# Optimization experiments

Measured on AMD Instinct MI355X. Metric: run time of the kernel, lower is better.

Reference implementation:

```python
import jax, jax.numpy as jnp
import numpy as np

BLKQ = 64
BLKK = 64
TOPK_RATIO = 0.25
EPS = 1e-05


def mean_pool(x, blk):
    B, H, L, D = x.shape
    return x.reshape(B, H, L // blk, blk, D).mean(axis=3)


def setup_inputs() -> dict:
    key = jax.random.key(0)
    kq, kk, kv, kw, kb = jax.random.split(key, 5)
    B, H, Lq, Lk, D = 1, 8, 4096, 4096, 64
    q = jax.random.normal(kq, (B, H, Lq, D), dtype=jnp.float32)
    k = jax.random.normal(kk, (B, H, Lk, D), dtype=jnp.float32)
    v = jax.random.normal(kv, (B, H, Lk, D), dtype=jnp.float32)
    # proj_l is zero-initialized in the original; use small random weights so the
    # linear-attention branch contributes non-trivially to the output.
    proj_w = jax.random.normal(kw, (D, D), dtype=jnp.float32) * 0.02
    proj_b = jax.random.normal(kb, (D,), dtype=jnp.float32) * 0.02
    return {"q": q, "k": k, "v": v, "proj_w": proj_w, "proj_b": proj_b}


def reference(q, k, v, proj_w, proj_b):
    B, H, Lq, D = q.shape
    Lk = k.shape[2]
    nQ, nK = Lq // BLKQ, Lk // BLKK

    # ---- block-level top-k routing (get_block_map_cross) ----
    arg_k = k - k.mean(axis=-2, keepdims=True)
    pq = mean_pool(q, BLKQ)                      # (B,H,nQ,D)
    pk = mean_pool(arg_k, BLKK)                  # (B,H,nK,D)
    pooled_score = jnp.einsum('bhqd,bhkd->bhqk', pq, pk)  # (B,H,nQ,nK)
    topk = min(nK, max(1, int(TOPK_RATIO * nK)))
    lut = jax.lax.top_k(pooled_score, topk)[1]   # (B,H,nQ,topk) int32

    # ---- block-sparse cross attention (softmax over selected K blocks) ----
    qb = q.reshape(B, H, nQ, BLKQ, D)
    kb = k.reshape(B, H, nK, BLKK, D)
    vb = v.reshape(B, H, nK, BLKK, D)
    gather = jax.vmap(jax.vmap(lambda blocks, idx: blocks[idx]))  # over B,H
    kg = gather(kb, lut)                         # (B,H,nQ,topk,BLKK,D)
    vg = gather(vb, lut)                         # (B,H,nQ,topk,BLKK,D)
    scale = D ** -0.5
    s = jnp.einsum('bhnqd,bhntkd->bhnqtk', qb, kg) * scale
    s = s.reshape(B, H, nQ, BLKQ, topk * BLKK)
    p = jax.nn.softmax(s, axis=-1)
    o_s = jnp.einsum('bhnqt,bhntd->bhnqd', p, vg.reshape(B, H, nQ, topk * BLKK, D))
    o_s = o_s.reshape(B, H, Lq, D)

    # ---- linear attention branch (softmax feature map, tied q/k) ----
    qf = jax.nn.softmax(q, axis=-1)
    kf = jax.nn.softmax(k, axis=-1)
    kv = jnp.einsum('bhkd,bhke->bhde', kf, v)    # (B,H,D,D)
    denom = jnp.einsum('bhqd,bhd->bhq', qf, kf.sum(axis=2)) + EPS
    o_l = jnp.einsum('bhqd,bhde->bhqe', qf, kv) / denom[..., None]
    o_l = o_l @ proj_w.T + proj_b                # proj_l

    return o_s + o_l
```

## Files before the change

kernel.cpp:

```cpp
#include <hip/hip_runtime.h>
#include <math.h>

#define H 8
#define L 4096
#define D 64
#define NBLK 64
#define TOPK 16
#define EPS 1e-5f
#define LP 68

typedef unsigned short u16;
typedef unsigned int u32;
typedef __attribute__((ext_vector_type(8))) short bf16x8;
typedef __attribute__((ext_vector_type(16))) float f32x16;
typedef __attribute__((ext_vector_type(4))) u32 u32x4;

static __device__ __forceinline__ u16 f2bf(float x) {
  u32 u = __float_as_uint(x);
  u32 r = (u + 0x7fffu + ((u >> 16) & 1u)) >> 16;
  return (u16)r;
}
static __device__ __forceinline__ float bf2f(u16 h) {
  return __uint_as_float(((u32)h) << 16);
}
__device__ __forceinline__ float dot4f(float4 a, float4 b) {
  return a.x * b.x + a.y * b.y + a.z * b.z + a.w * b.w;
}

__global__ __launch_bounds__(256) void kvprep_kernel(
    const float* __restrict__ k, const float* __restrict__ v,
    u16* __restrict__ kpkb, u16* __restrict__ vpkb,
    float* __restrict__ pkp, float* __restrict__ part_kv,
    float* __restrict__ part_ks) {
  const int kb = blockIdx.x, h = blockIdx.y;
  __shared__ float kst[64 * LP];
  __shared__ float vst[64 * LP];
  __shared__ float red[4][64];
  const int t = threadIdx.x;

  {
    const float4* ksrc = (const float4*)(k + ((size_t)h * L + (size_t)kb * 64) * D);
    const float4* vsrc = (const float4*)(v + ((size_t)h * L + (size_t)kb * 64) * D);
#pragma unroll
    for (int i = 0; i < 4; ++i) {
      int flat = i * 256 + t;
      int row = flat >> 4, c4 = flat & 15;
      *(float4*)&kst[row * LP + c4 * 4] = ksrc[flat];
      *(float4*)&vst[row * LP + c4 * 4] = vsrc[flat];
    }
  }
  __syncthreads();

  {
    u16* rowbase = kpkb + ((size_t)h * L + (size_t)kb * 64) * 128;
#pragma unroll
    for (int pass = 0; pass < 2; ++pass) {
      const int key = pass * 32 + (t >> 3);
      const int sub = t & 7;
      float f[8];
#pragma unroll
      for (int e = 0; e < 8; ++e) f[e] = kst[key * LP + sub * 8 + e];
      u16 hi[8], lo[8];
#pragma unroll
      for (int e = 0; e < 8; ++e) {
        hi[e] = f2bf(f[e]);
        lo[e] = f2bf(f[e] - bf2f(hi[e]));
      }
      const int c = sub >> 1, g2 = sub & 1;
      u16* row = rowbase + (size_t)key * 128;
      const int sh = ((c * 4 + g2 * 2 + 0) ^ (key & 15)) * 8;
      const int sl = ((c * 4 + g2 * 2 + 1) ^ (key & 15)) * 8;
      uint4 vh = {(u32)hi[0] | ((u32)hi[1] << 16), (u32)hi[2] | ((u32)hi[3] << 16),
                  (u32)hi[4] | ((u32)hi[5] << 16), (u32)hi[6] | ((u32)hi[7] << 16)};
      uint4 vl = {(u32)lo[0] | ((u32)lo[1] << 16), (u32)lo[2] | ((u32)lo[3] << 16),
                  (u32)lo[4] | ((u32)lo[5] << 16), (u32)lo[6] | ((u32)lo[7] << 16)};
      *(uint4*)(row + sh) = vh;
      *(uint4*)(row + sl) = vl;
    }
  }

  {
    const int d = t & 63, rr = t >> 6;
    float s = 0.f;
#pragma unroll
    for (int i = 0; i < 16; ++i) s += kst[(rr * 16 + i) * LP + d];
    red[rr][d] = s;
  }
  __syncthreads();
  {
    const int d = t & 63, rr = t >> 6;
    if (rr == 0) {
      float tot = red[0][d] + red[1][d] + red[2][d] + red[3][d];
      pkp[((size_t)h * NBLK + kb) * D + d] = tot * (1.f / 64.f);
    }
  }

  {
    u16* base = vpkb + (((size_t)h * 64 + kb) * 64) * 128;
#pragma unroll
    for (int iter = 0; iter < 4; ++iter) {
      const int dim = iter * 16 + (t >> 4);
      const int s = t & 15;
      const int cgh = s ^ (dim & 15);
      const int c = cgh >> 2, g = (cgh >> 1) & 1, hl = cgh & 1;
      u16 o[8];
#pragma unroll
      for (int e = 0; e < 8; ++e) {
        const int key = 4 * g + (e & 3) + 8 * ((e >> 2) + 2 * (c & 1)) + 32 * (c >> 1);
        float val = vst[key * LP + dim];
        u16 hi = f2bf(val);
        o[e] = hl ? f2bf(val - bf2f(hi)) : hi;
      }
      uint4 pk4 = {(u32)o[0] | ((u32)o[1] << 16), (u32)o[2] | ((u32)o[3] << 16),
                   (u32)o[4] | ((u32)o[5] << 16), (u32)o[6] | ((u32)o[7] << 16)};
      *(uint4*)(base + (size_t)dim * 128 + s * 8) = pk4;
    }
  }

  if (t < 128) {
    const int row = t >> 1, half = t & 1;
    float4 kr[8];
#pragma unroll
    for (int i = 0; i < 8; ++i) kr[i] = *(float4*)&kst[row * LP + half * 32 + i * 4];
    float mxk = -INFINITY;
#pragma unroll
    for (int i = 0; i < 8; ++i)
      mxk = fmaxf(mxk, fmaxf(fmaxf(kr[i].x, kr[i].y), fmaxf(kr[i].z, kr[i].w)));
    mxk = fmaxf(mxk, __shfl_xor(mxk, 1));
    float smk = 0.f;
#pragma unroll
    for (int i = 0; i < 8; ++i) {
      kr[i].x = __expf(kr[i].x - mxk); kr[i].y = __expf(kr[i].y - mxk);
      kr[i].z = __expf(kr[i].z - mxk); kr[i].w = __expf(kr[i].w - mxk);
      smk += kr[i].x + kr[i].y + kr[i].z + kr[i].w;
    }
    smk += __shfl_xor(smk, 1);
    const float inv = 1.f / smk;
#pragma unroll
    for (int i = 0; i < 8; ++i) {
      float4 o = kr[i];
      o.x *= inv; o.y *= inv; o.z *= inv; o.w *= inv;
      *(float4*)&kst[row * LP + half * 32 + i * 4] = o;
    }
  }
  __syncthreads();

  {
    const int d = t & 63, eg = t >> 6;
    float4 acc0 = make_float4(0.f, 0.f, 0.f, 0.f);
    float4 acc1 = acc0, acc2 = acc0, acc3 = acc0;
    float ksacc = 0.f;
#pragma unroll 4
    for (int lr = 0; lr < 64; ++lr) {
      const float wv = kst[lr * LP + d];
      if (eg == 0) ksacc += wv;
      const float4* vr = (const float4*)&vst[lr * LP + eg * 16];
      float4 v0 = vr[0], v1 = vr[1], v2 = vr[2], v3 = vr[3];
      acc0.x += wv * v0.x; acc0.y += wv * v0.y; acc0.z += wv * v0.z; acc0.w += wv * v0.w;
      acc1.x += wv * v1.x; acc1.y += wv * v1.y; acc1.z += wv * v1.z; acc1.w += wv * v1.w;
      acc2.x += wv * v2.x; acc2.y += wv * v2.y; acc2.z += wv * v2.z; acc2.w += wv * v2.w;
      acc3.x += wv * v3.x; acc3.y += wv * v3.y; acc3.z += wv * v3.z; acc3.w += wv * v3.w;
    }
    float* kvb = part_kv + ((size_t)(h * 64 + kb)) * 4096 + (size_t)d * 64 + eg * 16;
    *(float4*)(kvb + 0) = acc0;
    *(float4*)(kvb + 4) = acc1;
    *(float4*)(kvb + 8) = acc2;
    *(float4*)(kvb + 12) = acc3;
    if (eg == 0) part_ks[(size_t)(h * 64 + kb) * 64 + d] = ksacc;
  }
}

__global__ __launch_bounds__(256) void pool_kernel(
    const float* __restrict__ src, float* __restrict__ dst) {
  const int blk = blockIdx.x, h = blockIdx.y;
  const int d = threadIdx.x & 63, rr = threadIdx.x >> 6;
  const float* base = src + ((size_t)h * L + (size_t)blk * 64) * D;
  float s = 0.f;
#pragma unroll
  for (int i = 0; i < 16; ++i) s += base[(rr * 16 + i) * D + d];
  __shared__ float red[4][64];
  red[rr][d] = s;
  __syncthreads();
  if (rr == 0) {
    float tot = red[0][d] + red[1][d] + red[2][d] + red[3][d];
    dst[((size_t)h * NBLK + blk) * D + d] = tot * (1.f / 64.f);
  }
}

__global__ __launch_bounds__(64) void topk_kernel(
    const float* __restrict__ pq, const float* __restrict__ pk,
    int* __restrict__ lut) {
  const int qb = blockIdx.x, h = blockIdx.y;
  const int j = threadIdx.x;
  const float4* pqv = (const float4*)(pq + ((size_t)h * NBLK + qb) * D);
  const float4* pkv = (const float4*)(pk + ((size_t)h * NBLK + j) * D);
  float s = 0.f;
#pragma unroll
  for (int d4 = 0; d4 < 16; ++d4) s += dot4f(pqv[d4], pkv[d4]);
  int* lrow = lut + ((size_t)h * NBLK + qb) * TOPK;
  for (int t = 0; t < TOPK; ++t) {
    float m = s;
    int mi = j;
#pragma unroll
    for (int off = 32; off; off >>= 1) {
      float om = __shfl_xor(m, off);
      int omi = __shfl_xor(mi, off);
      if (om > m || (om == m && omi < mi)) { m = om; mi = omi; }
    }
    if (j == 0) lrow[t] = mi;
    if (j == mi) s = -INFINITY;
  }
}

__global__ __launch_bounds__(256, 4) void sattn_kernel(
    const float* __restrict__ q, const u16* __restrict__ kpk,
    const u16* __restrict__ vpk, const int* __restrict__ lut,
    float* __restrict__ out) {
  __shared__ alignas(16) char smem[32768];
  const int bx = blockIdx.x;
  const int h = bx & 7, qb = bx >> 3;
  const int t = threadIdx.x;
  const int lane = t & 63;
  const int ln = lane & 31;
  const int g = lane >> 5;
  const int w = t >> 6;
  const int p = w & 1;
  const int kh = w >> 1;

  float* qst = (float*)smem;
  {
    const float4* src = (const float4*)(q + ((size_t)h * L + (size_t)qb * 64) * D);
#pragma unroll
    for (int i = 0; i < 4; ++i) {
      int flat = i * 256 + t;
      *(float4*)&qst[(flat >> 4) * LP + (flat & 15) * 4] = src[flat];
    }
  }
  __syncthreads();
  bf16x8 qh[4], ql[4];
  {
    const int qrow = p * 32 + ln;
#pragma unroll
    for (int c = 0; c < 4; ++c) {
      const float* s8 = &qst[qrow * LP + c * 16 + g * 8];
#pragma unroll
      for (int e = 0; e < 8; ++e) {
        float x = s8[e] * 0.125f;
        u16 hi = f2bf(x);
        qh[c][e] = (short)hi;
        ql[c][e] = (short)f2bf(x - bf2f(hi));
      }
    }
  }
  __syncthreads();

  u16* KB = (u16*)smem;
  u16* VB = (u16*)smem + 8192;

  f32x16 o0, o1;
#pragma unroll
  for (int r = 0; r < 16; ++r) { o0[r] = 0.f; o1[r] = 0.f; }
  float lrun = 0.f;
  const int* lrow = lut + ((size_t)h * NBLK + qb) * TOPK;
  const int xr = ln & 15;
  const int krow = kh * 32 + ln;

  {
    const int kb = lrow[0];
    const uint4* gk = (const uint4*)(kpk + ((size_t)h * L + (size_t)kb * 64) * 128);
    const uint4* gv = (const uint4*)(vpk + (((size_t)h * 64 + kb) * 64) * 128);
    uint4* lk = (uint4*)KB;
    uint4* lv = (uint4*)VB;
#pragma unroll
    for (int i = 0; i < 4; ++i) {
      int x = i * 256 + t;
      lk[x] = gk[x];
      lv[x] = gv[x];
    }
  }
  __syncthreads();

  for (int ib = 0; ib < TOPK; ++ib) {
    f32x16 s0;
#pragma unroll
    for (int r = 0; r < 16; ++r) s0[r] = 0.f;
#pragma unroll
    for (int c = 0; c < 4; ++c) {
      const int sH = c * 4 + g * 2;
      bf16x8 k_h = *(const bf16x8*)(KB + (size_t)krow * 128 + ((sH ^ xr) * 8));
      bf16x8 k_l = *(const bf16x8*)(KB + (size_t)krow * 128 + (((sH + 1) ^ xr) * 8));
      s0 = __builtin_amdgcn_mfma_f32_32x32x16_bf16(k_h, qh[c], s0, 0, 0, 0);
      s0 = __builtin_amdgcn_mfma_f32_32x32x16_bf16(k_l, qh[c], s0, 0, 0, 0);
      s0 = __builtin_amdgcn_mfma_f32_32x32x16_bf16(k_h, ql[c], s0, 0, 0, 0);
    }

    u32 hpk[8], lpk[8];
    float psum = 0.f;
#pragma unroll
    for (int j = 0; j < 8; ++j) {
      float a = __expf(s0[2 * j]);
      float b = __expf(s0[2 * j + 1]);
      psum += a + b;
      u32 hp;
      asm("v_cvt_pk_bf16_f32 %0, %1, %2" : "=v"(hp) : "v"(a), "v"(b));
      hpk[j] = hp;
      float ah = __uint_as_float(hp << 16);
      float bh = __uint_as_float(hp & 0xffff0000u);
      u32 lp;
      asm("v_cvt_pk_bf16_f32 %0, %1, %2" : "=v"(lp) : "v"(a - ah), "v"(b - bh));
      lpk[j] = lp;
    }
    psum += __shfl_xor(psum, 32);
    lrun += psum;

#pragma unroll
    for (int cc = 0; cc < 2; ++cc) {
      union { u32x4 u; bf16x8 b; } ph, pl;
      ph.u = (u32x4){hpk[4 * cc + 0], hpk[4 * cc + 1], hpk[4 * cc + 2], hpk[4 * cc + 3]};
      pl.u = (u32x4){lpk[4 * cc + 0], lpk[4 * cc + 1], lpk[4 * cc + 2], lpk[4 * cc + 3]};
      const bf16x8 pah = ph.b, pal = pl.b;
      const int sH = (2 * kh + cc) * 4 + g * 2;
      bf16x8 v0h = *(const bf16x8*)(VB + (size_t)ln * 128 + ((sH ^ xr) * 8));
      bf16x8 v0l = *(const bf16x8*)(VB + (size_t)ln * 128 + (((sH + 1) ^ xr) * 8));
      bf16x8 v1h = *(const bf16x8*)(VB + (size_t)(32 + ln) * 128 + ((sH ^ xr) * 8));
      bf16x8 v1l = *(const bf16x8*)(VB + (size_t)(32 + ln) * 128 + (((sH + 1) ^ xr) * 8));
      o0 = __builtin_amdgcn_mfma_f32_32x32x16_bf16(pah, v0h, o0, 0, 0, 0);
      o0 = __builtin_amdgcn_mfma_f32_32x32x16_bf16(pal, v0h, o0, 0, 0, 0);
      o0 = __builtin_amdgcn_mfma_f32_32x32x16_bf16(pah, v0l, o0, 0, 0, 0);
      o1 = __builtin_amdgcn_mfma_f32_32x32x16_bf16(pah, v1h, o1, 0, 0, 0);
      o1 = __builtin_amdgcn_mfma_f32_32x32x16_bf16(pal, v1h, o1, 0, 0, 0);
      o1 = __builtin_amdgcn_mfma_f32_32x32x16_bf16(pah, v1l, o1, 0, 0, 0);
    }

    __syncthreads();
    if (ib + 1 < TOPK) {
      const int kb = lrow[ib + 1];
      const uint4* gk = (const uint4*)(kpk + ((size_t)h * L + (size_t)kb * 64) * 128);
      const uint4* gv = (const uint4*)(vpk + (((size_t)h * 64 + kb) * 64) * 128);
      uint4* lk = (uint4*)KB;
      uint4* lv = (uint4*)VB;
#pragma unroll
      for (int i = 0; i < 4; ++i) {
        int x = i * 256 + t;
        lk[x] = gk[x];
        lv[x] = gv[x];
      }
    }
    __syncthreads();
  }

  float* oxbase = (float*)smem;
  float* lxbase = (float*)smem + 4096;
  if (g == 0) lxbase[(p * 2 + kh) * 32 + ln] = lrun;
  if (kh == 1) {
#pragma unroll
    for (int r = 0; r < 16; ++r) {
      const int R = (r & 3) + 8 * (r >> 2) + 4 * g;
      oxbase[p * 2048 + R * 64 + ln] = o0[r];
      oxbase[p * 2048 + R * 64 + 32 + ln] = o1[r];
    }
  }
  __syncthreads();
  if (kh == 0) {
#pragma unroll
    for (int r = 0; r < 16; ++r) {
      const int R = (r & 3) + 8 * (r >> 2) + 4 * g;
      const float lt = lxbase[(p * 2 + 0) * 32 + R] + lxbase[(p * 2 + 1) * 32 + R];
      const float inv = 1.f / lt;
      const size_t row = (size_t)h * L + (size_t)qb * 64 + p * 32 + R;
      out[row * 64 + ln] = (o0[r] + oxbase[p * 2048 + R * 64 + ln]) * inv;
      out[row * 64 + 32 + ln] = (o1[r] + oxbase[p * 2048 + R * 64 + 32 + ln]) * inv;
    }
  }
}

__global__ __launch_bounds__(256) void kvred_kernel(
    const float* __restrict__ part_kv, const float* __restrict__ part_ks,
    float* __restrict__ p2kv, float* __restrict__ p2ks) {
  const int j = blockIdx.x, h = blockIdx.y;
  const int t = threadIdx.x;
  float4 s0 = make_float4(0.f, 0.f, 0.f, 0.f);
  float4 s1 = s0, s2 = s0, s3 = s0;
#pragma unroll
  for (int p = 0; p < 4; ++p) {
    const float4* src = (const float4*)(part_kv + ((size_t)(h * 64 + j * 4 + p)) * 4096);
    float4 a = src[0 * 256 + t], b = src[1 * 256 + t];
    float4 c = src[2 * 256 + t], d = src[3 * 256 + t];
    s0.x += a.x; s0.y += a.y; s0.z += a.z; s0.w += a.w;
    s1.x += b.x; s1.y += b.y; s1.z += b.z; s1.w += b.w;
    s2.x += c.x; s2.y += c.y; s2.z += c.z; s2.w += c.w;
    s3.x += d.x; s3.y += d.y; s3.z += d.z; s3.w += d.w;
  }
  float4* dst = (float4*)(p2kv + ((size_t)(h * 16 + j)) * 4096);
  dst[0 * 256 + t] = s0;
  dst[1 * 256 + t] = s1;
  dst[2 * 256 + t] = s2;
  dst[3 * 256 + t] = s3;
  if (t < 64) {
    float ks = 0.f;
#pragma unroll
    for (int p = 0; p < 4; ++p) ks += part_ks[(size_t)(h * 64 + j * 4 + p) * 64 + t];
    p2ks[(size_t)(h * 16 + j) * 64 + t] = ks;
  }
}

__global__ __launch_bounds__(256) void kvproj_kernel(
    const float* __restrict__ p2kv, const float* __restrict__ p2ks,
    const float* __restrict__ pw, float* __restrict__ kvp,
    float* __restrict__ ksum) {
  const int h = blockIdx.x;
  __shared__ float kvs[64 * 64];
  __shared__ float pws[64 * 64];
  const int t = threadIdx.x;
  float4 s0 = make_float4(0.f, 0.f, 0.f, 0.f);
  float4 s1 = s0, s2 = s0, s3 = s0;
  for (int p = 0; p < 16; ++p) {
    const float4* src = (const float4*)(p2kv + ((size_t)(h * 16 + p)) * 4096);
    float4 a = src[0 * 256 + t], b = src[1 * 256 + t];
    float4 cc = src[2 * 256 + t], dd = src[3 * 256 + t];
    s0.x += a.x; s0.y += a.y; s0.z += a.z; s0.w += a.w;
    s1.x += b.x; s1.y += b.y; s1.z += b.z; s1.w += b.w;
    s2.x += cc.x; s2.y += cc.y; s2.z += cc.z; s2.w += cc.w;
    s3.x += dd.x; s3.y += dd.y; s3.z += dd.z; s3.w += dd.w;
  }
  ((float4*)kvs)[0 * 256 + t] = s0;
  ((float4*)kvs)[1 * 256 + t] = s1;
  ((float4*)kvs)[2 * 256 + t] = s2;
  ((float4*)kvs)[3 * 256 + t] = s3;
#pragma unroll
  for (int i = 0; i < 4; ++i) {
    int f4 = i * 256 + t;
    ((float4*)pws)[f4] = ((const float4*)pw)[f4];
  }
  if (t < 64) {
    float ks = 0.f;
    for (int p = 0; p < 16; ++p) ks += p2ks[(size_t)(h * 16 + p) * 64 + t];
    ksum[(size_t)h * 64 + t] = ks;
  }
  __syncthreads();
  const int d = t & 63, fg = t >> 6;
  float* dst = kvp + (size_t)h * 4096 + (size_t)d * 64;
  const float4* a = (const float4*)&kvs[d * 64];
  for (int f = fg * 16; f < fg * 16 + 16; ++f) {
    const float4* b = (const float4*)&pws[f * 64];
    float s = 0.f;
#pragma unroll
    for (int e4 = 0; e4 < 16; ++e4) s += dot4f(a[e4], b[e4]);
    dst[f] = s;
  }
}

__global__ __launch_bounds__(256) void linattn_kernel(
    const float* __restrict__ q, const float* __restrict__ kvp,
    const float* __restrict__ ksum, const float* __restrict__ pb,
    float* __restrict__ out) {
  __shared__ float kvs[64 * 64];
  __shared__ float kss[64], pbs[64];
  const int t = threadIdx.x;
  const size_t grow = (size_t)blockIdx.x * 256 + t;
  const int h = (int)(grow >> 12);
#pragma unroll
  for (int i = 0; i < 4; ++i) {
    int f4 = i * 256 + t;
    ((float4*)kvs)[f4] = ((const float4*)(kvp + (size_t)h * 4096))[f4];
  }
  if (t < 64) {
    kss[t] = ksum[(size_t)h * 64 + t];
    pbs[t] = pb[t];
  }
  __syncthreads();
  const float* qrow = q + grow * 64;
  float mx = -INFINITY;
  const float4* q4p = (const float4*)qrow;
#pragma unroll
  for (int i = 0; i < 16; ++i) {
    float4 x = q4p[i];
    mx = fmaxf(mx, fmaxf(fmaxf(x.x, x.y), fmaxf(x.z, x.w)));
  }
  float4 tt[16];
#pragma unroll
  for (int i = 0; i < 16; ++i) tt[i] = make_float4(0.f, 0.f, 0.f, 0.f);
  float sm = 0.f, dn = 0.f;
#pragma unroll 4
  for (int dd = 0; dd < 64; ++dd) {
    const float wv = __expf(qrow[dd] - mx);
    sm += wv;
    dn += wv * kss[dd];
    const float4* kvr = (const float4*)&kvs[dd * 64];
#pragma unroll
    for (int e4 = 0; e4 < 16; ++e4) {
      float4 kk = kvr[e4];
      tt[e4].x += wv * kk.x; tt[e4].y += wv * kk.y;
      tt[e4].z += wv * kk.z; tt[e4].w += wv * kk.w;
    }
  }
  const float inv = 1.f / (dn + EPS * sm);
  float* orow = out + grow * 64;
#pragma unroll
  for (int e4 = 0; e4 < 16; ++e4) {
    float4 o = ((float4*)orow)[e4];
    o.x += tt[e4].x * inv + pbs[e4 * 4 + 0];
    o.y += tt[e4].y * inv + pbs[e4 * 4 + 1];
    o.z += tt[e4].z * inv + pbs[e4 * 4 + 2];
    o.w += tt[e4].w * inv + pbs[e4 * 4 + 3];
    ((float4*)orow)[e4] = o;
  }
}

extern "C" void kernel_launch(void* const* d_in, const int* in_sizes, int n_in,
                              void* d_out, int out_size, void* d_ws, size_t ws_size,
                              hipStream_t stream) {
  const float* q = (const float*)d_in[0];
  const float* k = (const float*)d_in[1];
  const float* v = (const float*)d_in[2];
  const float* pw = (const float*)d_in[3];
  const float* pb = (const float*)d_in[4];
  float* out = (float*)d_out;

  u16* kpkb = (u16*)d_ws;
  u16* vpkb = (u16*)d_ws + 4194304;
  float* fws = (float*)((char*)d_ws + 16777216);
  float* pq = fws;
  float* pk = fws + 32768;
  float* part_kv = fws + 65536;
  float* part_ks = fws + 2162688;
  float* p2kv = fws + 2195456;
  float* p2ks = fws + 2719744;
  float* kvp = fws + 2727936;
  float* ksum = fws + 2760704;
  int* lut = (int*)(fws + 2761216);

  kvprep_kernel<<<dim3(64, 8), 256, 0, stream>>>(k, v, kpkb, vpkb, pk, part_kv, part_ks);
  pool_kernel<<<dim3(64, 8), 256, 0, stream>>>(q, pq);
  topk_kernel<<<dim3(64, 8), 64, 0, stream>>>(pq, pk, lut);
  sattn_kernel<<<512, 256, 0, stream>>>(q, kpkb, vpkb, lut, out);
  kvred_kernel<<<dim3(16, 8), 256, 0, stream>>>(part_kv, part_ks, p2kv, p2ks);
  kvproj_kernel<<<8, 256, 0, stream>>>(p2kv, p2ks, pw, kvp, ksum);
  linattn_kernel<<<128, 256, 0, stream>>>(q, kvp, ksum, pb, out);
}
```

Measured before the change: 177.2 us.

## Double-buffer K/V blocks with async global-to-LDS loads in sparse attention

The sparse-attention kernel now prefetches the next selected K/V block into a second LDS buffer with async global_load_lds copies while the current block is computed, replacing the load-then-compute pattern that used two barriers per step. LDS per block doubles to 64KB and the launch-bounds occupancy hint drops from 4 to 2 blocks. It also loads Q straight from global memory into registers instead of staging it through LDS, and raises wave priority around the MFMA sections. This lowers achievable occupancy, though with 512 blocks on the device that may already be near the actual residency.

Result: faster. 172.0 us (-2.9%).

```diff
diff --git a/kernel.cpp b/kernel.cpp
--- a/kernel.cpp
+++ b/kernel.cpp
@@ -25,6 +25,11 @@
 }
 __device__ __forceinline__ float dot4f(float4 a, float4 b) {
   return a.x * b.x + a.y * b.y + a.z * b.z + a.w * b.w;
+}
+static __device__ __forceinline__ void async_cp16(uint4* lds, const uint4* g) {
+  __builtin_amdgcn_global_load_lds(
+      (const __attribute__((address_space(1))) void*)g,
+      (__attribute__((address_space(3))) void*)lds, 16, 0, 0);
 }
 
 __global__ __launch_bounds__(256) void kvprep_kernel(
@@ -212,11 +217,11 @@
   }
 }
 
-__global__ __launch_bounds__(256, 4) void sattn_kernel(
+__global__ __launch_bounds__(256, 2) void sattn_kernel(
     const float* __restrict__ q, const u16* __restrict__ kpk,
     const u16* __restrict__ vpk, const int* __restrict__ lut,
     float* __restrict__ out) {
-  __shared__ alignas(16) char smem[32768];
+  __shared__ alignas(16) char smem[65536];
   const int bx = blockIdx.x;
   const int h = bx & 7, qb = bx >> 3;
   const int t = threadIdx.x;
@@ -227,35 +232,26 @@
   const int p = w & 1;
   const int kh = w >> 1;
 
-  float* qst = (float*)smem;
-  {
-    const float4* src = (const float4*)(q + ((size_t)h * L + (size_t)qb * 64) * D);
-#pragma unroll
-    for (int i = 0; i < 4; ++i) {
-      int flat = i * 256 + t;
-      *(float4*)&qst[(flat >> 4) * LP + (flat & 15) * 4] = src[flat];
-    }
-  }
-  __syncthreads();
   bf16x8 qh[4], ql[4];
   {
-    const int qrow = p * 32 + ln;
+    const float* qrowp = q + ((size_t)h * L + (size_t)qb * 64 + p * 32 + ln) * D;
 #pragma unroll
     for (int c = 0; c < 4; ++c) {
-      const float* s8 = &qst[qrow * LP + c * 16 + g * 8];
+      float4 a = *(const float4*)(qrowp + c * 16 + g * 8);
+      float4 b = *(const float4*)(qrowp + c * 16 + g * 8 + 4);
+      float f[8] = {a.x, a.y, a.z, a.w, b.x, b.y, b.z, b.w};
 #pragma unroll
       for (int e = 0; e < 8; ++e) {
-        float x = s8[e] * 0.125f;
+        float x = f[e] * 0.125f;
         u16 hi = f2bf(x);
         qh[c][e] = (short)hi;
         ql[c][e] = (short)f2bf(x - bf2f(hi));
       }
     }
   }
-  __syncthreads();
-
-  u16* KB = (u16*)smem;
-  u16* VB = (u16*)smem + 8192;
+
+  u16* bufA = (u16*)smem;
+  u16* bufB = (u16*)smem + 16384;
 
   f32x16 o0, o1;
 #pragma unroll
@@ -265,25 +261,35 @@
   const int xr = ln & 15;
   const int krow = kh * 32 + ln;
 
-  {
-    const int kb = lrow[0];
-    const uint4* gk = (const uint4*)(kpk + ((size_t)h * L + (size_t)kb * 64) * 128);
-    const uint4* gv = (const uint4*)(vpk + (((size_t)h * 64 + kb) * 64) * 128);
-    uint4* lk = (uint4*)KB;
-    uint4* lv = (uint4*)VB;
-#pragma unroll
-    for (int i = 0; i < 4; ++i) {
-      int x = i * 256 + t;
-      lk[x] = gk[x];
-      lv[x] = gv[x];
-    }
-  }
-  __syncthreads();
-
+#define STAGE(dst, kbi)                                                        \
+  {                                                                            \
+    const int kb_ = (kbi);                                                     \
+    const uint4* gk = (const uint4*)(kpk + ((size_t)h * L + (size_t)kb_ * 64) * 128); \
+    const uint4* gv = (const uint4*)(vpk + (((size_t)h * 64 + kb_) * 64) * 128);      \
+    uint4* lk = (uint4*)(dst);                                                 \
+    uint4* lv = (uint4*)((dst) + 8192);                                        \
+    _Pragma("unroll") for (int i_ = 0; i_ < 4; ++i_) {                         \
+      int x_ = i_ * 256 + t;                                                   \
+      async_cp16(lk + x_, gk + x_);                                            \
+      async_cp16(lv + x_, gv + x_);                                            \
+    }                                                                          \
+  }
+
+  STAGE(bufA, lrow[0]);
+  __syncthreads();
+
+  u16* cur = bufA;
+  u16* nxt = bufB;
   for (int ib = 0; ib < TOPK; ++ib) {
+    if (ib + 1 < TOPK) STAGE(nxt, lrow[ib + 1]);
+
+    const u16* KB = cur;
+    const u16* VB = cur + 8192;
+
     f32x16 s0;
 #pragma unroll
     for (int r = 0; r < 16; ++r) s0[r] = 0.f;
+    __builtin_amdgcn_s_setprio(1);
 #pragma unroll
     for (int c = 0; c < 4; ++c) {
       const int sH = c * 4 + g * 2;
@@ -293,6 +299,7 @@
       s0 = __builtin_amdgcn_mfma_f32_32x32x16_bf16(k_l, qh[c], s0, 0, 0, 0);
       s0 = __builtin_amdgcn_mfma_f32_32x32x16_bf16(k_h, ql[c], s0, 0, 0, 0);
     }
+    __builtin_amdgcn_s_setprio(0);
 
     u32 hpk[8], lpk[8];
     float psum = 0.f;
@@ -313,6 +320,7 @@
     psum += __shfl_xor(psum, 32);
     lrun += psum;
 
+    __builtin_amdgcn_s_setprio(1);
 #pragma unroll
     for (int cc = 0; cc < 2; ++cc) {
       union { u32x4 u; bf16x8 b; } ph, pl;
@@ -331,23 +339,12 @@
       o1 = __builtin_amdgcn_mfma_f32_32x32x16_bf16(pal, v1h, o1, 0, 0, 0);
       o1 = __builtin_amdgcn_mfma_f32_32x32x16_bf16(pah, v1l, o1, 0, 0, 0);
     }
+    __builtin_amdgcn_s_setprio(0);
 
     __syncthreads();
-    if (ib + 1 < TOPK) {
-      const int kb = lrow[ib + 1];
-      const uint4* gk = (const uint4*)(kpk + ((size_t)h * L + (size_t)kb * 64) * 128);
-      const uint4* gv = (const uint4*)(vpk + (((size_t)h * 64 + kb) * 64) * 128);
-      uint4* lk = (uint4*)KB;
-      uint4* lv = (uint4*)VB;
-#pragma unroll
-      for (int i = 0; i < 4; ++i) {
-        int x = i * 256 + t;
-        lk[x] = gk[x];
-        lv[x] = gv[x];
-      }
-    }
-    __syncthreads();
-  }
+    u16* tmp = cur; cur = nxt; nxt = tmp;
+  }
+#undef STAGE
 
   float* oxbase = (float*)smem;
   float* lxbase = (float*)smem + 4096;
```
